# Kernel optimization log

Hardware: AMD Instinct MI355X
Metric: run time of the kernel (lower is better)

## Reference

```python
import jax, jax.numpy as jnp
import numpy as np

D, NH, K = 768, 12, 2
B, T = 4, 2048
DH = D // NH
SCALE = float(np.sqrt(DH))


def setup_inputs() -> dict:
    key = jax.random.key(0)
    ks = jax.random.split(key, 9)
    H = jax.random.normal(ks[0], (B, T, D), dtype=jnp.float32)
    p = jax.random.uniform(ks[1], (B, T, K), dtype=jnp.float32)
    p = p / jnp.sum(p, axis=-1, keepdims=True)  # language probabilities
    s = jax.random.uniform(ks[2], (B, T), dtype=jnp.float32)
    w_init = 0.02
    wq = w_init * jax.random.normal(ks[3], (D, D), dtype=jnp.float32)
    wk = w_init * jax.random.normal(ks[4], (D, D), dtype=jnp.float32)
    wv = w_init * jax.random.normal(ks[5], (D, D), dtype=jnp.float32)
    wo = w_init * jax.random.normal(ks[6], (D, D), dtype=jnp.float32)
    bo = jnp.zeros((D,), dtype=jnp.float32)
    # per-head KxK compat matrices, init identity + small noise (as in torch code)
    compat = (jnp.broadcast_to(jnp.eye(K, dtype=jnp.float32), (NH, K, K))
              + 0.01 * jax.random.normal(ks[7], (NH, K, K), dtype=jnp.float32))
    gamma = 0.1 * jax.random.normal(ks[8], (1,), dtype=jnp.float32)
    return {"H": H, "p": p, "s": s, "wq": wq, "wk": wk, "wv": wv,
            "wo": wo, "bo": bo, "compat": compat, "gamma": gamma}


def _split(x):
    # (B,T,D) -> (B,NH,T,DH)
    b, t, _ = x.shape
    return x.reshape(b, t, NH, DH).transpose(0, 2, 1, 3)


def reference(H, p, s, wq, wk, wv, wo, bo, compat, gamma):
    # torch nn.Linear: y = x @ W.T  (weights stored (out,in))
    Q = _split(jnp.einsum('btd,ed->bte', H, wq))
    Kt = _split(jnp.einsum('btd,ed->bte', H, wk))
    V = _split(jnp.einsum('btd,ed->bte', H, wv))
    scores = jnp.einsum('bhid,bhjd->bhij', Q, Kt) / SCALE            # (B,H,T,T)
    p_compat = jnp.einsum('bik,hkl->bhil', p, compat)                 # (B,H,T,K)
    scores = scores + jnp.einsum('bhil,bjl->bhij', p_compat, p)       # bilinear lang bias
    scores = scores + gamma[0] * s[:, None, None, :]                  # position bias
    attn = jax.nn.softmax(scores, axis=-1)                            # dropout p=0 (eval)
    ctx = jnp.einsum('bhij,bhjd->bhid', attn, V)
    merged = ctx.transpose(0, 2, 1, 3).reshape(H.shape[0], H.shape[1], D)
    return jnp.einsum('btd,ed->bte', merged, wo) + bo
```

## Files before the change

kernel.cpp:

```cpp
#include <hip/hip_runtime.h>
#include <stdint.h>

#define TT 2048
#define DD 768
#define NHEAD 12
#define DH 64
#define MM 8192
#define DP 80

typedef __attribute__((ext_vector_type(8))) short bf16x8;
typedef __attribute__((ext_vector_type(4))) float f32x4;
typedef __attribute__((ext_vector_type(16))) float f32x16;
typedef __attribute__((ext_vector_type(2))) unsigned int u32x2v;
typedef unsigned short u16;

#define GAS __attribute__((address_space(1)))
#define LAS __attribute__((address_space(3)))

static __device__ __forceinline__ void gload16(const void* g, void* l) {
  __builtin_amdgcn_global_load_lds((const GAS uint32_t*)g, (LAS uint32_t*)l, 16, 0, 0);
}

static __device__ __forceinline__ u16 f2b(float f) {
  union { float f; uint32_t u; } x; x.f = f;
  uint32_t r = x.u + 0x7fffu + ((x.u >> 16) & 1u);
  return (u16)(r >> 16);
}
static __device__ __forceinline__ float b2f(u16 v) {
  union { uint32_t u; float f; } x; x.u = ((uint32_t)v) << 16; return x.f;
}

#if __has_builtin(__builtin_amdgcn_exp2f)
#define EXP2(x) __builtin_amdgcn_exp2f(x)
#else
#define EXP2(x) exp2f(x)
#endif

static __device__ __forceinline__ void pswap(uint32_t& a, uint32_t& b) {
#if __has_builtin(__builtin_amdgcn_permlane32_swap)
  u32x2v r = __builtin_amdgcn_permlane32_swap(a, b, false, false);
  a = r[0]; b = r[1];
#else
  uint32_t ax = (uint32_t)__shfl_xor((int)a, 32, 64);
  uint32_t bx = (uint32_t)__shfl_xor((int)b, 32, 64);
  bool lo = (threadIdx.x & 32) == 0;
  uint32_t na = lo ? a : bx, nb = lo ? ax : b;
  a = na; b = nb;
#endif
}
static __device__ __forceinline__ uint32_t cvtpk(float lo, float hi_) {
  uint32_t r;
  asm("v_cvt_pk_bf16_f32 %0, %1, %2" : "=v"(r) : "v"(lo), "v"(hi_));
  return r;
}
static __device__ __forceinline__ f32x16 mfma32(bf16x8 a, bf16x8 b, f32x16 c) {
  return __builtin_amdgcn_mfma_f32_32x32x16_bf16(a, b, c, 0, 0, 0);
}

__global__ __launch_bounds__(256) void convert_kernel(
    const float* __restrict__ H, const float* __restrict__ wq,
    const float* __restrict__ wk, const float* __restrict__ wv,
    const float* __restrict__ wo,
    u16* __restrict__ Hb, u16* __restrict__ Wqkv, u16* __restrict__ Wob) {
  const size_t NHEL = (size_t)MM * DD;
  const size_t NW = (size_t)DD * DD;
  size_t i = ((size_t)blockIdx.x * 256 + threadIdx.x) * 4;
  const float* src; u16* dst; size_t so, dofs;
  if (i < NHEL) { src = H; so = i; dst = Hb; dofs = i; }
  else if (i < NHEL + 3 * NW) {
    size_t j = i - NHEL; dst = Wqkv; dofs = j;
    if (j < NW) { src = wq; so = j; }
    else if (j < 2 * NW) { src = wk; so = j - NW; }
    else { src = wv; so = j - 2 * NW; }
  } else if (i < NHEL + 4 * NW) {
    size_t j = i - NHEL - 3 * NW; src = wo; so = j; dst = Wob; dofs = j;
  } else return;
  float4 v = *(const float4*)&src[so];
  ushort4 o;
  o.x = f2b(v.x); o.y = f2b(v.y); o.z = f2b(v.z); o.w = f2b(v.w);
  *(ushort4*)&dst[dofs] = o;
}

template <int MODE>
__global__ __launch_bounds__(256) void gemm_kernel(
    const u16* __restrict__ A, const u16* __restrict__ Bw,
    u16* __restrict__ Qp, u16* __restrict__ Kp, u16* __restrict__ Vt,
    const float* __restrict__ bo, float* __restrict__ Out) {
  __shared__ u16 SMEM[17408];
  u16* As = SMEM;
  u16* Bs = SMEM + 8192;
  const int tid = threadIdx.x;
  const int lane = tid & 63, w = tid >> 6;
  const int wr = w >> 1, wc = w & 1;
  const int g = lane >> 4, r = lane & 15;
  const int m0 = blockIdx.x * 128, n0 = blockIdx.y * 128;

  f32x4 acc[4][4];
#pragma unroll
  for (int m = 0; m < 4; ++m)
#pragma unroll
    for (int n = 0; n < 4; ++n) acc[m][n] = (f32x4){0.f, 0.f, 0.f, 0.f};

  for (int ks = 0; ks < 12; ++ks) {
    const int k0 = ks * 64;
    __syncthreads();
#pragma unroll
    for (int ii = 0; ii < 4; ++ii) {
      int seg = (w * 4 + ii) * 64 + lane;
      int row = seg >> 3, cs = seg & 7;
      int csw = cs ^ (row & 7);
      gload16(&A[(size_t)(m0 + row) * DD + k0 + csw * 8], &As[(w * 4 + ii) * 512]);
      gload16(&Bw[(size_t)(n0 + row) * DD + k0 + csw * 8], &Bs[(w * 4 + ii) * 512]);
    }
    __syncthreads();
#pragma unroll
    for (int kk = 0; kk < 2; ++kk) {
      bf16x8 af[4], bfr[4];
#pragma unroll
      for (int m = 0; m < 4; ++m) {
        int row = wr * 64 + m * 16 + r;
        int ch = (kk * 4 + g) ^ (row & 7);
        af[m] = *(const bf16x8*)&As[row * 64 + ch * 8];
      }
#pragma unroll
      for (int n = 0; n < 4; ++n) {
        int row = wc * 64 + n * 16 + r;
        int ch = (kk * 4 + g) ^ (row & 7);
        bfr[n] = *(const bf16x8*)&Bs[row * 64 + ch * 8];
      }
#pragma unroll
      for (int m = 0; m < 4; ++m)
#pragma unroll
        for (int n = 0; n < 4; ++n)
          acc[m][n] = __builtin_amdgcn_mfma_f32_16x16x32_bf16(af[m], bfr[n], acc[m][n], 0, 0, 0);
    }
  }

  if (MODE == 0) {
    const int sel = n0 / DD;
    const int e0b = n0 - sel * DD;
    const int bb = m0 >> 11;
    const int tb = m0 & (TT - 1);
    __syncthreads();
#pragma unroll
    for (int m = 0; m < 4; ++m) {
#pragma unroll
      for (int n = 0; n < 4; ++n) {
#pragma unroll
        for (int reg = 0; reg < 4; ++reg) {
          float v = acc[m][n][reg];
          int t = wr * 64 + m * 16 + g * 4 + reg;
          int c = wc * 64 + n * 16 + r;
          u16 bv = f2b(sel == 0 ? v * 0.18033688f : v);
          if (sel < 2) SMEM[t * 136 + c] = bv;
          else         SMEM[c * 136 + t] = bv;
        }
      }
    }
    __syncthreads();
    if (sel < 2) {
      u16* base = (sel == 0) ? Qp : Kp;
      const int grp = tid >> 3, li = tid & 7;
#pragma unroll
      for (int it = 0; it < 8; ++it) {
        int chunk = it * 32 + grp;
        int t = chunk & 127, hh = chunk >> 7;
        int h = (e0b >> 6) + hh;
        size_t row = ((size_t)(bb * NHEAD + h) * TT + tb + t) * DP;
        uint4 d = *(const uint4*)&SMEM[t * 136 + hh * 64 + li * 8];
        *(uint4*)&base[row + li * 8] = d;
      }
    } else {
      const int grp = tid >> 4, li = tid & 15;
#pragma unroll
      for (int it = 0; it < 8; ++it) {
        int c = it * 16 + grp;
        int h = (e0b >> 6) + (c >> 6), dh = c & 63;
        size_t row = ((size_t)(bb * NHEAD + h)) * DH * TT + (size_t)dh * TT + tb;
        uint4 d = *(const uint4*)&SMEM[c * 136 + li * 8];
        *(uint4*)&Vt[row + li * 8] = d;
      }
    }
  } else {
#pragma unroll
    for (int m = 0; m < 4; ++m) {
#pragma unroll
      for (int n = 0; n < 4; ++n) {
#pragma unroll
        for (int reg = 0; reg < 4; ++reg) {
          int gt = m0 + wr * 64 + m * 16 + g * 4 + reg;
          int e = n0 + wc * 64 + n * 16 + r;
          Out[(size_t)gt * DD + e] = acc[m][n][reg] + bo[e];
        }
      }
    }
  }
}

__global__ __launch_bounds__(256) void bias_fill(
    const float* __restrict__ p, const float* __restrict__ s,
    const float* __restrict__ compat, const float* __restrict__ gamma,
    u16* __restrict__ Qp, u16* __restrict__ Kp) {
  int i = blockIdx.x * 256 + threadIdx.x;
  if (i >= MM) return;
  int b = i >> 11, t = i & (TT - 1);
  const float L2E = 1.44269504f;
  float p0 = p[(size_t)i * 2], p1 = p[(size_t)i * 2 + 1], sv = s[i];
  u16 p0h = f2b(p0); u16 p0l = f2b(p0 - b2f(p0h));
  u16 p1h = f2b(p1); u16 p1l = f2b(p1 - b2f(p1h));
  u16 svh = f2b(sv); u16 svl = f2b(sv - b2f(svh));
  u16 gmb = f2b(gamma[0] * L2E);
  union { u16 u[8]; uint4 v; } kv, qv, zz;
#pragma unroll
  for (int z = 0; z < 8; ++z) zz.u[z] = 0;
  kv.u[0] = p0h; kv.u[1] = p0l; kv.u[2] = p1h; kv.u[3] = p1l;
  kv.u[4] = svh; kv.u[5] = svl; kv.u[6] = 0; kv.u[7] = 0;
#pragma unroll
  for (int h = 0; h < NHEAD; ++h) {
    float c00 = compat[h * 4 + 0], c01 = compat[h * 4 + 1];
    float c10 = compat[h * 4 + 2], c11 = compat[h * 4 + 3];
    u16 q0 = f2b((p0 * c00 + p1 * c10) * L2E);
    u16 q1 = f2b((p0 * c01 + p1 * c11) * L2E);
    qv.u[0] = q0; qv.u[1] = q0; qv.u[2] = q1; qv.u[3] = q1;
    qv.u[4] = gmb; qv.u[5] = gmb; qv.u[6] = 0; qv.u[7] = 0;
    size_t row = ((size_t)(b * NHEAD + h) * TT + t) * DP;
    *(uint4*)&Qp[row + 64] = qv.v;
    *(uint4*)&Qp[row + 72] = zz.v;
    *(uint4*)&Kp[row + 64] = kv.v;
    *(uint4*)&Kp[row + 72] = zz.v;
  }
}

#define QB 128
__global__ __launch_bounds__(256, 3) void attn_kernel(
    const u16* __restrict__ Qp, const u16* __restrict__ Kp, const u16* __restrict__ Vtb,
    u16* __restrict__ Ctx) {
  __shared__ u16 Ks[2][64 * 88];
  __shared__ u16 Vs[2][64 * 64];
  const int tid = threadIdx.x, lane = tid & 63, w = tid >> 6;
  const int hi = lane >> 5, ql = lane & 31;
  const int bid = blockIdx.x;
  const int bh = bid % 48, qb = bid / 48;
  const int b = bh / NHEAD, h = bh % NHEAD;

  const char* KgB = (const char*)(Kp + (size_t)bh * TT * DP);
  const char* VgB = (const char*)(Vtb + (size_t)bh * DH * TT);
  const u16* Qg = Qp + (size_t)bh * TT * DP;

  const int q = qb * QB + w * 32 + ql;
  bf16x8 Qf[5];
#pragma unroll
  for (int kbl = 0; kbl < 5; ++kbl)
    Qf[kbl] = *(const bf16x8*)&Qg[(size_t)q * DP + (2 * kbl + hi) * 8];

  union { u16 u[8]; bf16x8 v; } ones;
#pragma unroll
  for (int z = 0; z < 8; ++z) ones.u[z] = 0x3F80;

  auto kofs = [&](int i) {
    int n = i * 64 + lane;
    int rr = (n * 2979) >> 15;
    int c = n - 11 * rr; if (c > 9) c = 9;
    return rr * 160 + c * 16;
  };
  auto vofs = [&](int j) {
    int n = j * 64 + lane;
    int dh = n >> 3, cs = n & 7;
    return dh * 4096 + (cs ^ (dh & 7)) * 16;
  };
  const int koff0 = kofs(w), koff1 = kofs(w + 4), koff2 = (w < 3) ? kofs(w + 8) : 0;
  const int voff0 = vofs(w), voff1 = vofs(w + 4);

  auto STAGE = [&](int nb, int t0) {
    const char* ksrc = KgB + (size_t)t0 * 160;
    char* kd = (char*)&Ks[nb][0];
    gload16(ksrc + koff0, kd + w * 1024);
    gload16(ksrc + koff1, kd + (w + 4) * 1024);
    if (w < 3) gload16(ksrc + koff2, kd + (w + 8) * 1024);
    const char* vsrc = VgB + (size_t)t0 * 2;
    char* vd = (char*)&Vs[nb][0];
    gload16(vsrc + voff0, vd + w * 1024);
    gload16(vsrc + voff1, vd + (w + 4) * 1024);
  };

  f32x16 o0, o1, ol;
#pragma unroll
  for (int z = 0; z < 16; ++z) { o0[z] = 0.f; o1[z] = 0.f; ol[z] = 0.f; }

  STAGE(0, 0);

  for (int kt = 0; kt < 32; ++kt) {
    __syncthreads();
    if (kt + 1 < 32) STAGE((kt + 1) & 1, (kt + 1) * 64);
    const u16* Kb_ = &Ks[kt & 1][0];
    const u16* Vb_ = &Vs[kt & 1][0];

    f32x16 s0, s1;
#pragma unroll
    for (int z = 0; z < 16; ++z) { s0[z] = 0.f; s1[z] = 0.f; }
    __builtin_amdgcn_s_setprio(1);
#pragma unroll
    for (int kbl = 0; kbl < 5; ++kbl) {
      bf16x8 a0 = *(const bf16x8*)&Kb_[ql * 88 + hi * 8 + kbl * 16];
      s0 = mfma32(a0, Qf[kbl], s0);
    }
#pragma unroll
    for (int kbl = 0; kbl < 5; ++kbl) {
      bf16x8 a1 = *(const bf16x8*)&Kb_[(ql + 32) * 88 + hi * 8 + kbl * 16];
      s1 = mfma32(a1, Qf[kbl], s1);
    }
    __builtin_amdgcn_s_setprio(0);

    float p_[32];
#pragma unroll
    for (int z = 0; z < 16; ++z) p_[z] = EXP2(s0[z]);
#pragma unroll
    for (int z = 0; z < 16; ++z) p_[16 + z] = EXP2(s1[z]);

    __builtin_amdgcn_s_setprio(1);
#pragma unroll
    for (int ks = 0; ks < 4; ++ks) {
      const int base = ks * 8;
      uint32_t wa = cvtpk(p_[base + 0], p_[base + 1]);
      uint32_t wb = cvtpk(p_[base + 4], p_[base + 5]);
      uint32_t wc = cvtpk(p_[base + 2], p_[base + 3]);
      uint32_t wd = cvtpk(p_[base + 6], p_[base + 7]);
      pswap(wa, wb);
      pswap(wc, wd);
      union { uint32_t u[4]; bf16x8 v; } pa;
      pa.u[0] = wa; pa.u[1] = wc; pa.u[2] = wb; pa.u[3] = wd;
#pragma unroll
      for (int nb = 0; nb < 2; ++nb) {
        int row = ql + 32 * nb;
        bf16x8 vf = *(const bf16x8*)&Vb_[row * 64 + (((2 * ks + hi) ^ (ql & 7)) * 8)];
        if (nb == 0) o0 = mfma32(pa.v, vf, o0);
        else         o1 = mfma32(pa.v, vf, o1);
      }
      ol = mfma32(pa.v, ones.v, ol);
    }
    __builtin_amdgcn_s_setprio(0);
  }

#pragma unroll
  for (int z = 0; z < 16; ++z) {
    int q2 = (z & 3) + 8 * (z >> 2) + 4 * hi;
    float il = 1.0f / ol[z];
    int qrow = qb * QB + w * 32 + q2;
    size_t rowb = ((size_t)b * TT + qrow) * DD + h * DH;
    Ctx[rowb + ql]      = f2b(o0[z] * il);
    Ctx[rowb + ql + 32] = f2b(o1[z] * il);
  }
}

extern "C" void kernel_launch(void* const* d_in, const int* in_sizes, int n_in,
                              void* d_out, int out_size, void* d_ws, size_t ws_size,
                              hipStream_t stream) {
  const float* H = (const float*)d_in[0];
  const float* p = (const float*)d_in[1];
  const float* s = (const float*)d_in[2];
  const float* wq = (const float*)d_in[3];
  const float* wk = (const float*)d_in[4];
  const float* wv = (const float*)d_in[5];
  const float* wo = (const float*)d_in[6];
  const float* bo = (const float*)d_in[7];
  const float* compat = (const float*)d_in[8];
  const float* gamma = (const float*)d_in[9];
  float* out = (float*)d_out;

  char* ws = (char*)d_ws;
  u16* Hb   = (u16*)(ws);
  u16* Wqkv = (u16*)(ws + 12582912);
  u16* Wob  = (u16*)(ws + 16121856);
  u16* Qpb  = (u16*)(ws + 17301504);
  u16* Kpb  = (u16*)(ws + 33030144);
  u16* Vtb  = (u16*)(ws + 48758784);
  u16* Ctx  = Hb;

  convert_kernel<<<8448, 256, 0, stream>>>(H, wq, wk, wv, wo, Hb, Wqkv, Wob);
  gemm_kernel<0><<<dim3(64, 18), 256, 0, stream>>>(Hb, Wqkv, Qpb, Kpb, Vtb, nullptr, nullptr);
  bias_fill<<<32, 256, 0, stream>>>(p, s, compat, gamma, Qpb, Kpb);
  attn_kernel<<<768, 256, 0, stream>>>(Qpb, Kpb, Vtb, Ctx);
  gemm_kernel<1><<<dim3(64, 6), 256, 0, stream>>>(Ctx, Wob, nullptr, nullptr, nullptr, bo, out);
}
```

Measured before the change: 162.5 us.

## Give each attention wave two query tiles and fold bias fill into convert

The attention kernel moves from four waves of 32 queries each to two waves of 64 queries each. Every K and V fragment read from LDS now feeds two query tiles, which halves LDS reads per MFMA and raises MFMA density per wave. The cost is more accumulator registers, fewer waves per block and lower occupancy, with launch_bounds changed to (128,2). The separate bias_fill kernel becomes extra blocks of the convert kernel, which removes one launch and now runs before the QKV GEMM instead of after it.

```diff
diff --git a/kernel.cpp b/kernel.cpp
--- a/kernel.cpp
+++ b/kernel.cpp
@@ -61,9 +61,43 @@
     const float* __restrict__ H, const float* __restrict__ wq,
     const float* __restrict__ wk, const float* __restrict__ wv,
     const float* __restrict__ wo,
-    u16* __restrict__ Hb, u16* __restrict__ Wqkv, u16* __restrict__ Wob) {
+    const float* __restrict__ p, const float* __restrict__ s,
+    const float* __restrict__ compat, const float* __restrict__ gamma,
+    u16* __restrict__ Hb, u16* __restrict__ Wqkv, u16* __restrict__ Wob,
+    u16* __restrict__ Qp, u16* __restrict__ Kp) {
   const size_t NHEL = (size_t)MM * DD;
   const size_t NW = (size_t)DD * DD;
+  if (blockIdx.x >= 8448) {
+    int i = (blockIdx.x - 8448) * 256 + threadIdx.x;
+    if (i >= MM) return;
+    int b = i >> 11, t = i & (TT - 1);
+    const float L2E = 1.44269504f;
+    float p0 = p[(size_t)i * 2], p1 = p[(size_t)i * 2 + 1], sv = s[i];
+    u16 p0h = f2b(p0); u16 p0l = f2b(p0 - b2f(p0h));
+    u16 p1h = f2b(p1); u16 p1l = f2b(p1 - b2f(p1h));
+    u16 svh = f2b(sv); u16 svl = f2b(sv - b2f(svh));
+    u16 gmb = f2b(gamma[0] * L2E);
+    union { u16 u[8]; uint4 v; } kv, qv, zz;
+#pragma unroll
+    for (int z = 0; z < 8; ++z) zz.u[z] = 0;
+    kv.u[0] = p0h; kv.u[1] = p0l; kv.u[2] = p1h; kv.u[3] = p1l;
+    kv.u[4] = svh; kv.u[5] = svl; kv.u[6] = 0; kv.u[7] = 0;
+#pragma unroll
+    for (int h = 0; h < NHEAD; ++h) {
+      float c00 = compat[h * 4 + 0], c01 = compat[h * 4 + 1];
+      float c10 = compat[h * 4 + 2], c11 = compat[h * 4 + 3];
+      u16 q0 = f2b((p0 * c00 + p1 * c10) * L2E);
+      u16 q1 = f2b((p0 * c01 + p1 * c11) * L2E);
+      qv.u[0] = q0; qv.u[1] = q0; qv.u[2] = q1; qv.u[3] = q1;
+      qv.u[4] = gmb; qv.u[5] = gmb; qv.u[6] = 0; qv.u[7] = 0;
+      size_t row = ((size_t)(b * NHEAD + h) * TT + t) * DP;
+      *(uint4*)&Qp[row + 64] = qv.v;
+      *(uint4*)&Qp[row + 72] = zz.v;
+      *(uint4*)&Kp[row + 64] = kv.v;
+      *(uint4*)&Kp[row + 72] = zz.v;
+    }
+    return;
+  }
   size_t i = ((size_t)blockIdx.x * 256 + threadIdx.x) * 4;
   const float* src; u16* dst; size_t so, dofs;
   if (i < NHEL) { src = H; so = i; dst = Hb; dofs = i; }
@@ -197,42 +231,8 @@
   }
 }
 
-__global__ __launch_bounds__(256) void bias_fill(
-    const float* __restrict__ p, const float* __restrict__ s,
-    const float* __restrict__ compat, const float* __restrict__ gamma,
-    u16* __restrict__ Qp, u16* __restrict__ Kp) {
-  int i = blockIdx.x * 256 + threadIdx.x;
-  if (i >= MM) return;
-  int b = i >> 11, t = i & (TT - 1);
-  const float L2E = 1.44269504f;
-  float p0 = p[(size_t)i * 2], p1 = p[(size_t)i * 2 + 1], sv = s[i];
-  u16 p0h = f2b(p0); u16 p0l = f2b(p0 - b2f(p0h));
-  u16 p1h = f2b(p1); u16 p1l = f2b(p1 - b2f(p1h));
-  u16 svh = f2b(sv); u16 svl = f2b(sv - b2f(svh));
-  u16 gmb = f2b(gamma[0] * L2E);
-  union { u16 u[8]; uint4 v; } kv, qv, zz;
-#pragma unroll
-  for (int z = 0; z < 8; ++z) zz.u[z] = 0;
-  kv.u[0] = p0h; kv.u[1] = p0l; kv.u[2] = p1h; kv.u[3] = p1l;
-  kv.u[4] = svh; kv.u[5] = svl; kv.u[6] = 0; kv.u[7] = 0;
-#pragma unroll
-  for (int h = 0; h < NHEAD; ++h) {
-    float c00 = compat[h * 4 + 0], c01 = compat[h * 4 + 1];
-    float c10 = compat[h * 4 + 2], c11 = compat[h * 4 + 3];
-    u16 q0 = f2b((p0 * c00 + p1 * c10) * L2E);
-    u16 q1 = f2b((p0 * c01 + p1 * c11) * L2E);
-    qv.u[0] = q0; qv.u[1] = q0; qv.u[2] = q1; qv.u[3] = q1;
-    qv.u[4] = gmb; qv.u[5] = gmb; qv.u[6] = 0; qv.u[7] = 0;
-    size_t row = ((size_t)(b * NHEAD + h) * TT + t) * DP;
-    *(uint4*)&Qp[row + 64] = qv.v;
-    *(uint4*)&Qp[row + 72] = zz.v;
-    *(uint4*)&Kp[row + 64] = kv.v;
-    *(uint4*)&Kp[row + 72] = zz.v;
-  }
-}
-
-#define QB 128
-__global__ __launch_bounds__(256, 3) void attn_kernel(
+#define QBLK 128
+__global__ __launch_bounds__(128, 2) void attn_kernel(
     const u16* __restrict__ Qp, const u16* __restrict__ Kp, const u16* __restrict__ Vtb,
     u16* __restrict__ Ctx) {
   __shared__ u16 Ks[2][64 * 88];
@@ -247,45 +247,49 @@
   const char* VgB = (const char*)(Vtb + (size_t)bh * DH * TT);
   const u16* Qg = Qp + (size_t)bh * TT * DP;
 
-  const int q = qb * QB + w * 32 + ql;
-  bf16x8 Qf[5];
-#pragma unroll
-  for (int kbl = 0; kbl < 5; ++kbl)
-    Qf[kbl] = *(const bf16x8*)&Qg[(size_t)q * DP + (2 * kbl + hi) * 8];
+  const int q0r = qb * QBLK + w * 64 + ql;
+  bf16x8 Qf0[5], Qf1[5];
+#pragma unroll
+  for (int kbl = 0; kbl < 5; ++kbl) {
+    Qf0[kbl] = *(const bf16x8*)&Qg[(size_t)q0r * DP + (2 * kbl + hi) * 8];
+    Qf1[kbl] = *(const bf16x8*)&Qg[(size_t)(q0r + 32) * DP + (2 * kbl + hi) * 8];
+  }
 
   union { u16 u[8]; bf16x8 v; } ones;
 #pragma unroll
   for (int z = 0; z < 8; ++z) ones.u[z] = 0x3F80;
-
-  auto kofs = [&](int i) {
-    int n = i * 64 + lane;
-    int rr = (n * 2979) >> 15;
-    int c = n - 11 * rr; if (c > 9) c = 9;
-    return rr * 160 + c * 16;
-  };
-  auto vofs = [&](int j) {
-    int n = j * 64 + lane;
-    int dh = n >> 3, cs = n & 7;
-    return dh * 4096 + (cs ^ (dh & 7)) * 16;
-  };
-  const int koff0 = kofs(w), koff1 = kofs(w + 4), koff2 = (w < 3) ? kofs(w + 8) : 0;
-  const int voff0 = vofs(w), voff1 = vofs(w + 4);
 
   auto STAGE = [&](int nb, int t0) {
     const char* ksrc = KgB + (size_t)t0 * 160;
     char* kd = (char*)&Ks[nb][0];
-    gload16(ksrc + koff0, kd + w * 1024);
-    gload16(ksrc + koff1, kd + (w + 4) * 1024);
-    if (w < 3) gload16(ksrc + koff2, kd + (w + 8) * 1024);
+#pragma unroll
+    for (int i = 0; i < 5; ++i) {
+      int n = (i * 2 + w) * 64 + lane;
+      int rr = (n * 2979) >> 15;
+      int c = n - 11 * rr; if (c > 9) c = 9;
+      gload16(ksrc + rr * 160 + c * 16, kd + (i * 2 + w) * 1024);
+    }
+    if (w == 0) {
+      int n = 640 + lane;
+      int rr = (n * 2979) >> 15;
+      int c = n - 11 * rr; if (c > 9) c = 9;
+      gload16(ksrc + rr * 160 + c * 16, kd + 10240);
+    }
     const char* vsrc = VgB + (size_t)t0 * 2;
     char* vd = (char*)&Vs[nb][0];
-    gload16(vsrc + voff0, vd + w * 1024);
-    gload16(vsrc + voff1, vd + (w + 4) * 1024);
+#pragma unroll
+    for (int j = 0; j < 4; ++j) {
+      int n = (j * 2 + w) * 64 + lane;
+      int dh = n >> 3, cs = n & 7;
+      gload16(vsrc + dh * 4096 + ((cs ^ (dh & 7))) * 16, vd + (j * 2 + w) * 1024);
+    }
   };
 
-  f32x16 o0, o1, ol;
-#pragma unroll
-  for (int z = 0; z < 16; ++z) { o0[z] = 0.f; o1[z] = 0.f; ol[z] = 0.f; }
+  f32x16 o00, o01, o10, o11, ol0, ol1;
+#pragma unroll
+  for (int z = 0; z < 16; ++z) {
+    o00[z] = 0.f; o01[z] = 0.f; o10[z] = 0.f; o11[z] = 0.f; ol0[z] = 0.f; ol1[z] = 0.f;
+  }
 
   STAGE(0, 0);
 
@@ -295,48 +299,59 @@
     const u16* Kb_ = &Ks[kt & 1][0];
     const u16* Vb_ = &Vs[kt & 1][0];
 
-    f32x16 s0, s1;
-#pragma unroll
-    for (int z = 0; z < 16; ++z) { s0[z] = 0.f; s1[z] = 0.f; }
+    f32x16 s00, s01, s10, s11;
+#pragma unroll
+    for (int z = 0; z < 16; ++z) { s00[z] = 0.f; s01[z] = 0.f; s10[z] = 0.f; s11[z] = 0.f; }
     __builtin_amdgcn_s_setprio(1);
 #pragma unroll
     for (int kbl = 0; kbl < 5; ++kbl) {
-      bf16x8 a0 = *(const bf16x8*)&Kb_[ql * 88 + hi * 8 + kbl * 16];
-      s0 = mfma32(a0, Qf[kbl], s0);
-    }
-#pragma unroll
-    for (int kbl = 0; kbl < 5; ++kbl) {
-      bf16x8 a1 = *(const bf16x8*)&Kb_[(ql + 32) * 88 + hi * 8 + kbl * 16];
-      s1 = mfma32(a1, Qf[kbl], s1);
+      bf16x8 kf0 = *(const bf16x8*)&Kb_[ql * 88 + hi * 8 + kbl * 16];
+      bf16x8 kf1 = *(const bf16x8*)&Kb_[(ql + 32) * 88 + hi * 8 + kbl * 16];
+      s00 = mfma32(kf0, Qf0[kbl], s00);
+      s01 = mfma32(kf0, Qf1[kbl], s01);
+      s10 = mfma32(kf1, Qf0[kbl], s10);
+      s11 = mfma32(kf1, Qf1[kbl], s11);
     }
     __builtin_amdgcn_s_setprio(0);
 
-    float p_[32];
-#pragma unroll
-    for (int z = 0; z < 16; ++z) p_[z] = EXP2(s0[z]);
-#pragma unroll
-    for (int z = 0; z < 16; ++z) p_[16 + z] = EXP2(s1[z]);
+    bf16x8 pa0[4], pa1[4];
+#pragma unroll
+    for (int half = 0; half < 2; ++half) {
+      float p_[32];
+      if (half == 0) {
+#pragma unroll
+        for (int z = 0; z < 16; ++z) { p_[z] = EXP2(s00[z]); p_[16 + z] = EXP2(s10[z]); }
+      } else {
+#pragma unroll
+        for (int z = 0; z < 16; ++z) { p_[z] = EXP2(s01[z]); p_[16 + z] = EXP2(s11[z]); }
+      }
+#pragma unroll
+      for (int ks = 0; ks < 4; ++ks) {
+        const int base = ks * 8;
+        uint32_t wa = cvtpk(p_[base + 0], p_[base + 1]);
+        uint32_t wb = cvtpk(p_[base + 4], p_[base + 5]);
+        uint32_t wc = cvtpk(p_[base + 2], p_[base + 3]);
+        uint32_t wd = cvtpk(p_[base + 6], p_[base + 7]);
+        pswap(wa, wb);
+        pswap(wc, wd);
+        union { uint32_t u[4]; bf16x8 v; } pa;
+        pa.u[0] = wa; pa.u[1] = wc; pa.u[2] = wb; pa.u[3] = wd;
+        if (half == 0) pa0[ks] = pa.v; else pa1[ks] = pa.v;
+      }
+    }
 
     __builtin_amdgcn_s_setprio(1);
 #pragma unroll
     for (int ks = 0; ks < 4; ++ks) {
-      const int base = ks * 8;
-      uint32_t wa = cvtpk(p_[base + 0], p_[base + 1]);
-      uint32_t wb = cvtpk(p_[base + 4], p_[base + 5]);
-      uint32_t wc = cvtpk(p_[base + 2], p_[base + 3]);
-      uint32_t wd = cvtpk(p_[base + 6], p_[base + 7]);
-      pswap(wa, wb);
-      pswap(wc, wd);
-      union { uint32_t u[4]; bf16x8 v; } pa;
-      pa.u[0] = wa; pa.u[1] = wc; pa.u[2] = wb; pa.u[3] = wd;
-#pragma unroll
-      for (int nb = 0; nb < 2; ++nb) {
-        int row = ql + 32 * nb;
-        bf16x8 vf = *(const bf16x8*)&Vb_[row * 64 + (((2 * ks + hi) ^ (ql & 7)) * 8)];
-        if (nb == 0) o0 = mfma32(pa.v, vf, o0);
-        else         o1 = mfma32(pa.v, vf, o1);
-      }
-      ol = mfma32(pa.v, ones.v, ol);
+      const int sw = ((2 * ks + hi) ^ (ql & 7)) * 8;
+      bf16x8 vf0 = *(const bf16x8*)&Vb_[ql * 64 + sw];
+      bf16x8 vf1 = *(const bf16x8*)&Vb_[(ql + 32) * 64 + sw];
+      o00 = mfma32(pa0[ks], vf0, o00);
+      o10 = mfma32(pa1[ks], vf0, o10);
+      o01 = mfma32(pa0[ks], vf1, o01);
+      o11 = mfma32(pa1[ks], vf1, o11);
+      ol0 = mfma32(pa0[ks], ones.v, ol0);
+      ol1 = mfma32(pa1[ks], ones.v, ol1);
     }
     __builtin_amdgcn_s_setprio(0);
   }
@@ -344,11 +359,15 @@
 #pragma unroll
   for (int z = 0; z < 16; ++z) {
     int q2 = (z & 3) + 8 * (z >> 2) + 4 * hi;
-    float il = 1.0f / ol[z];
-    int qrow = qb * QB + w * 32 + q2;
-    size_t rowb = ((size_t)b * TT + qrow) * DD + h * DH;
-    Ctx[rowb + ql]      = f2b(o0[z] * il);
-    Ctx[rowb + ql + 32] = f2b(o1[z] * il);
+    int qrow0 = qb * QBLK + w * 64 + q2;
+    float il0 = 1.0f / ol0[z];
+    size_t rowb0 = ((size_t)b * TT + qrow0) * DD + h * DH;
+    Ctx[rowb0 + ql]      = f2b(o00[z] * il0);
+    Ctx[rowb0 + ql + 32] = f2b(o01[z] * il0);
+    float il1 = 1.0f / ol1[z];
+    size_t rowb1 = rowb0 + 32 * DD;
+    Ctx[rowb1 + ql]      = f2b(o10[z] * il1);
+    Ctx[rowb1 + ql + 32] = f2b(o11[z] * il1);
   }
 }
 
@@ -376,9 +395,9 @@
   u16* Vtb  = (u16*)(ws + 48758784);
   u16* Ctx  = Hb;
 
-  convert_kernel<<<8448, 256, 0, stream>>>(H, wq, wk, wv, wo, Hb, Wqkv, Wob);
+  convert_kernel<<<8480, 256, 0, stream>>>(H, wq, wk, wv, wo, p, s, compat, gamma,
+                                           Hb, Wqkv, Wob, Qpb, Kpb);
   gemm_kernel<0><<<dim3(64, 18), 256, 0, stream>>>(Hb, Wqkv, Qpb, Kpb, Vtb, nullptr, nullptr);
-  bias_fill<<<32, 256, 0, stream>>>(p, s, compat, gamma, Qpb, Kpb);
-  attn_kernel<<<768, 256, 0, stream>>>(Qpb, Kpb, Vtb, Ctx);
+  attn_kernel<<<768, 128, 0, stream>>>(Qpb, Kpb, Vtb, Ctx);
   gemm_kernel<1><<<dim3(64, 6), 256, 0, stream>>>(Ctx, Wob, nullptr, nullptr, nullptr, bo, out);
 }
```

Result: slower. 169.0 us (+4.0%).
